# Performance work log

Measured on AMD Instinct MI355X. Metric: run time of the kernel, lower is better.

The kernel has to match this reference:

```python
import jax, jax.numpy as jnp
import numpy as np

B = 131072      # batch
NC = 1000       # num_classes
A = 128         # action_dim
ELD = 128       # embedding_latent_dim
VQN = 512       # vq_num_embeddings
VQD = 64        # vq_embedding_dim
SQUISH = 1.0
CC = 0.25       # commitment cost

def _he(k, fi, fo):
    lim = float(np.sqrt(6.0 / fi))
    return jax.random.uniform(k, (fi, fo), jnp.float32, -lim, lim)

def setup_inputs() -> dict:
    key = jax.random.key(0)
    ks = jax.random.split(key, 16)
    cb_lim = float(np.sqrt(3.0 / VQD))  # variance_scaling fan_in uniform
    return {
        "obs": jax.random.randint(ks[0], (B,), 0, NC),
        "embed": jax.random.normal(ks[1], (NC, ELD), jnp.float32) * 0.02,
        "W1": _he(ks[2], ELD, 128), "b1": jnp.zeros((128,), jnp.float32),
        "W2": _he(ks[3], 128, 128), "b2": jnp.zeros((128,), jnp.float32),
        "W3": _he(ks[4], 128, 128), "b3": jnp.zeros((128,), jnp.float32),
        "Wp": _he(ks[5], 128, VQD), "bp": jnp.zeros((VQD,), jnp.float32),
        "codebook": jax.random.uniform(ks[6], (VQN, VQD), jnp.float32, -cb_lim, cb_lim),
        "Wa": jax.random.normal(ks[7], (VQD, A), jnp.float32) * 0.01, "ba": jnp.zeros((A,), jnp.float32),
        "Ws": jax.random.normal(ks[8], (VQD, A), jnp.float32) * 0.01, "bs": jnp.zeros((A,), jnp.float32),
        "Wc1": _he(ks[9], VQD, 128), "bc1": jnp.zeros((128,), jnp.float32),
        "Wc2": _he(ks[10], 128, 128), "bc2": jnp.zeros((128,), jnp.float32),
        "Wc3": _he(ks[11], 128, 32), "bc3": jnp.zeros((32,), jnp.float32),
        "Wc4": _he(ks[12], 32, 1), "bc4": jnp.zeros((1,), jnp.float32),
    }

def reference(obs, embed, W1, b1, W2, b2, W3, b3, Wp, bp, codebook,
              Wa, ba, Ws, bs, Wc1, bc1, Wc2, bc2, Wc3, bc3, Wc4, bc4):
    # embedding lookup + small dense stack
    y = jnp.take(embed, obs, axis=0)                 # [B, 128]
    z = jax.nn.relu(y @ W1 + b1)
    z = jax.nn.relu(z @ W2 + b2)
    z = jax.nn.relu(z @ W3 + b3)
    z = z @ Wp + bp                                  # [B, 64] project to vq dim
    # VQ: pairwise squared distances, argmin, gather (== one_hot @ codebook)
    d = (jnp.sum(z * z, axis=1, keepdims=True)
         - 2.0 * (z @ codebook.T)
         + jnp.sum(codebook * codebook, axis=1))     # [B, 512]
    idx = jnp.argmin(d, axis=1)                      # [B]
    quant = jnp.take(codebook, idx, axis=0)          # [B, 64]
    q = z + jax.lax.stop_gradient(quant - z)         # straight-through
    e_loss = jnp.mean((jax.lax.stop_gradient(q) - z) ** 2)
    q_loss = jnp.mean((q - jax.lax.stop_gradient(z)) ** 2)
    vq_loss = q_loss + CC * e_loss
    # actor heads (pi = MvNormalDiag(actor_mean, scale_diag); return params)
    actor_mean = jax.nn.sigmoid(q @ Wa + ba)
    scale_diag = jax.nn.sigmoid(q @ Ws + bs) * SQUISH + 1e-8
    # critic head
    c = jax.nn.sigmoid(q @ Wc1 + bc1)
    c = jax.nn.sigmoid(c @ Wc2 + bc2)
    c = jax.nn.sigmoid(c @ Wc3 + bc3)
    critic = jnp.squeeze(c @ Wc4 + bc4, axis=-1)     # [B]
    return actor_mean, scale_diag, critic, vq_loss, idx
```

## Files before the change

kernel.cpp:

```cpp
#include <hip/hip_runtime.h>
#include <math.h>


typedef float f4 __attribute__((ext_vector_type(4)));

__device__ __forceinline__ float sigmoidf_(float x){ return 1.0f/(1.0f + expf(-x)); }

__global__ __launch_bounds__(128) void per_class_kernel(
    const float* __restrict__ embed,
    const float* __restrict__ W1, const float* __restrict__ b1,
    const float* __restrict__ W2, const float* __restrict__ b2,
    const float* __restrict__ W3, const float* __restrict__ b3,
    const float* __restrict__ Wp, const float* __restrict__ bp,
    const float* __restrict__ cb,
    const float* __restrict__ Wa, const float* __restrict__ ba,
    const float* __restrict__ Ws, const float* __restrict__ bs,
    const float* __restrict__ Wc1, const float* __restrict__ bc1,
    const float* __restrict__ Wc2, const float* __restrict__ bc2,
    const float* __restrict__ Wc3, const float* __restrict__ bc3,
    const float* __restrict__ Wc4, const float* __restrict__ bc4,
    float* __restrict__ am_t, float* __restrict__ sd_t,
    float* __restrict__ cr_t, int* __restrict__ idx_t, float* __restrict__ e_t,
    float* __restrict__ loss_slot, int VQN)
{
    const int c = blockIdx.x;
    const int t = threadIdx.x;
    if (c == 0 && t == 0) *loss_slot = 0.0f;

    __shared__ double Abuf[128];
    __shared__ double Bbuf[128];
    __shared__ double zp[64];
    __shared__ float  qv[64];
    __shared__ double rd[128];
    __shared__ int    ri[128];
    __shared__ float  h1[128], h2[128], h3[32];

    Abuf[t] = (double)embed[(size_t)c * 128 + t];
    __syncthreads();

    {
        double a0 = (double)b1[t], a1 = 0.0, a2 = 0.0, a3 = 0.0;
        for (int i = 0; i < 128; i += 4) {
            a0 = fma(Abuf[i+0], (double)W1[(i+0) * 128 + t], a0);
            a1 = fma(Abuf[i+1], (double)W1[(i+1) * 128 + t], a1);
            a2 = fma(Abuf[i+2], (double)W1[(i+2) * 128 + t], a2);
            a3 = fma(Abuf[i+3], (double)W1[(i+3) * 128 + t], a3);
        }
        double acc = (a0 + a1) + (a2 + a3);
        Bbuf[t] = acc > 0.0 ? acc : 0.0;
    }
    __syncthreads();

    {
        double a0 = (double)b2[t], a1 = 0.0, a2 = 0.0, a3 = 0.0;
        for (int i = 0; i < 128; i += 4) {
            a0 = fma(Bbuf[i+0], (double)W2[(i+0) * 128 + t], a0);
            a1 = fma(Bbuf[i+1], (double)W2[(i+1) * 128 + t], a1);
            a2 = fma(Bbuf[i+2], (double)W2[(i+2) * 128 + t], a2);
            a3 = fma(Bbuf[i+3], (double)W2[(i+3) * 128 + t], a3);
        }
        double acc = (a0 + a1) + (a2 + a3);
        Abuf[t] = acc > 0.0 ? acc : 0.0;
    }
    __syncthreads();

    {
        double a0 = (double)b3[t], a1 = 0.0, a2 = 0.0, a3 = 0.0;
        for (int i = 0; i < 128; i += 4) {
            a0 = fma(Abuf[i+0], (double)W3[(i+0) * 128 + t], a0);
            a1 = fma(Abuf[i+1], (double)W3[(i+1) * 128 + t], a1);
            a2 = fma(Abuf[i+2], (double)W3[(i+2) * 128 + t], a2);
            a3 = fma(Abuf[i+3], (double)W3[(i+3) * 128 + t], a3);
        }
        double acc = (a0 + a1) + (a2 + a3);
        Bbuf[t] = acc > 0.0 ? acc : 0.0;
    }
    __syncthreads();

    if (t < 64) {
        double a0 = (double)bp[t], a1 = 0.0, a2 = 0.0, a3 = 0.0;
        for (int i = 0; i < 128; i += 4) {
            a0 = fma(Bbuf[i+0], (double)Wp[(i+0) * 64 + t], a0);
            a1 = fma(Bbuf[i+1], (double)Wp[(i+1) * 64 + t], a1);
            a2 = fma(Bbuf[i+2], (double)Wp[(i+2) * 64 + t], a2);
            a3 = fma(Bbuf[i+3], (double)Wp[(i+3) * 64 + t], a3);
        }
        zp[t] = (a0 + a1) + (a2 + a3);
    }
    __syncthreads();

    double best = 1e300; int bidx = 0;
    for (int k = t; k < VQN; k += 128) {
        const float* crow = cb + (size_t)k * 64;
        double s0 = 0.0, s1 = 0.0;
        for (int j = 0; j < 64; j += 2) {
            double d0 = zp[j+0] - (double)crow[j+0];
            double d1 = zp[j+1] - (double)crow[j+1];
            s0 = fma(d0, d0, s0);
            s1 = fma(d1, d1, s1);
        }
        double s = s0 + s1;
        if (s < best) { best = s; bidx = k; }
    }
    rd[t] = best; ri[t] = bidx;
    __syncthreads();
    for (int sft = 64; sft > 0; sft >>= 1) {
        if (t < sft) {
            if (rd[t + sft] < rd[t] || (rd[t + sft] == rd[t] && ri[t + sft] < ri[t])) {
                rd[t] = rd[t + sft]; ri[t] = ri[t + sft];
            }
        }
        __syncthreads();
    }
    const int widx = ri[0];
    if (t < 64) qv[t] = cb[(size_t)widx * 64 + t];
    __syncthreads();

    {
        float la0 = ba[t],  la1 = 0.0f;
        float ls0 = bs[t],  ls1 = 0.0f;
        float l10 = bc1[t], l11 = 0.0f;
        for (int j = 0; j < 64; j += 2) {
            float q0 = qv[j], q1 = qv[j+1];
            la0 = fmaf(q0, Wa[j * 128 + t], la0);
            la1 = fmaf(q1, Wa[(j+1) * 128 + t], la1);
            ls0 = fmaf(q0, Ws[j * 128 + t], ls0);
            ls1 = fmaf(q1, Ws[(j+1) * 128 + t], ls1);
            l10 = fmaf(q0, Wc1[j * 128 + t], l10);
            l11 = fmaf(q1, Wc1[(j+1) * 128 + t], l11);
        }
        am_t[(size_t)c * 128 + t] = sigmoidf_(la0 + la1);
        sd_t[(size_t)c * 128 + t] = sigmoidf_(ls0 + ls1) * 1.0f + 1e-8f;
        h1[t] = sigmoidf_(l10 + l11);
    }
    __syncthreads();

    {
        float l20 = bc2[t], l21 = 0.0f;
        for (int i = 0; i < 128; i += 2) {
            l20 = fmaf(h1[i],   Wc2[i * 128 + t],     l20);
            l21 = fmaf(h1[i+1], Wc2[(i+1) * 128 + t], l21);
        }
        h2[t] = sigmoidf_(l20 + l21);
    }
    __syncthreads();

    if (t < 32) {
        float l30 = bc3[t], l31 = 0.0f;
        for (int i = 0; i < 128; i += 2) {
            l30 = fmaf(h2[i],   Wc3[i * 32 + t],     l30);
            l31 = fmaf(h2[i+1], Wc3[(i+1) * 32 + t], l31);
        }
        h3[t] = sigmoidf_(l30 + l31);
    }
    __syncthreads();

    if (t == 0) {
        float l4 = bc4[0];
        for (int i = 0; i < 32; ++i) l4 = fmaf(h3[i], Wc4[i], l4);
        cr_t[c] = l4;
        idx_t[c] = widx;
        double e0 = 0.0, e1 = 0.0;
        for (int j = 0; j < 64; j += 2) {
            double d0 = (double)qv[j]   - zp[j];
            double d1 = (double)qv[j+1] - zp[j+1];
            e0 = fma(d0, d0, e0); e1 = fma(d1, d1, e1);
        }
        e_t[c] = (float)(e0 + e1);
    }
}

__global__ __launch_bounds__(256) void scatter_vec_kernel(
    const int* __restrict__ obs,
    const f4* __restrict__ am_t, const f4* __restrict__ sd_t,
    f4* __restrict__ out, int B)
{
    int gid = blockIdx.x * 256 + threadIdx.x;
    int half = B * 32;
    if (gid < half) {
        int b = gid >> 5;
        int j = gid & 31;
        __builtin_nontemporal_store(am_t[(size_t)obs[b] * 32 + j], &out[gid]);
    } else {
        int g = gid - half;
        int b = g >> 5;
        int j = g & 31;
        __builtin_nontemporal_store(sd_t[(size_t)obs[b] * 32 + j], &out[gid]);
    }
}

__global__ __launch_bounds__(256) void scatter_scalar_kernel(
    const int* __restrict__ obs, const float* __restrict__ cr_t,
    const int* __restrict__ idx_t, const float* __restrict__ e_t,
    float* __restrict__ out_critic, float* __restrict__ out_idx,
    float* __restrict__ out_loss, int B, float scale)
{
    int b = blockIdx.x * 256 + threadIdx.x;
    float e = 0.0f;
    if (b < B) {
        int o = obs[b];
        __builtin_nontemporal_store(cr_t[o], &out_critic[b]);
        __builtin_nontemporal_store((float)idx_t[o], &out_idx[b]);
        e = e_t[o];
    }
    __shared__ float red[256];
    red[threadIdx.x] = e;
    __syncthreads();
    for (int s = 128; s > 0; s >>= 1) {
        if (threadIdx.x < s) red[threadIdx.x] += red[threadIdx.x + s];
        __syncthreads();
    }
    if (threadIdx.x == 0) atomicAdd(out_loss, red[0] * scale);
}

extern "C" void kernel_launch(void* const* d_in, const int* in_sizes, int n_in,
                              void* d_out, int out_size, void* d_ws, size_t ws_size,
                              hipStream_t stream)
{
    const int*   obs   = (const int*)  d_in[0];
    const float* embed = (const float*)d_in[1];
    const float* W1    = (const float*)d_in[2];
    const float* b1    = (const float*)d_in[3];
    const float* W2    = (const float*)d_in[4];
    const float* b2    = (const float*)d_in[5];
    const float* W3    = (const float*)d_in[6];
    const float* b3    = (const float*)d_in[7];
    const float* Wp    = (const float*)d_in[8];
    const float* bp    = (const float*)d_in[9];
    const float* cb    = (const float*)d_in[10];
    const float* Wa    = (const float*)d_in[11];
    const float* ba    = (const float*)d_in[12];
    const float* Ws    = (const float*)d_in[13];
    const float* bs    = (const float*)d_in[14];
    const float* Wc1   = (const float*)d_in[15];
    const float* bc1   = (const float*)d_in[16];
    const float* Wc2   = (const float*)d_in[17];
    const float* bc2   = (const float*)d_in[18];
    const float* Wc3   = (const float*)d_in[19];
    const float* bc3   = (const float*)d_in[20];
    const float* Wc4   = (const float*)d_in[21];
    const float* bc4   = (const float*)d_in[22];

    const int B   = in_sizes[0];
    const int NC  = in_sizes[1] / 128;
    const int VQN = in_sizes[10] / 64;

    float* am_t = (float*)d_ws;
    float* sd_t = am_t + (size_t)NC * 128;
    float* cr_t = sd_t + (size_t)NC * 128;
    float* e_t  = cr_t + NC;
    int*   idx_t = (int*)(e_t + NC);

    float* out = (float*)d_out;
    const size_t cr_off   = (size_t)B * 256;
    const size_t loss_off = cr_off + (size_t)B;
    const size_t idx_off  = loss_off + 1;

    per_class_kernel<<<NC, 128, 0, stream>>>(
        embed, W1, b1, W2, b2, W3, b3, Wp, bp, cb,
        Wa, ba, Ws, bs, Wc1, bc1, Wc2, bc2, Wc3, bc3, Wc4, bc4,
        am_t, sd_t, cr_t, idx_t, e_t, out + loss_off, VQN);

    int vec_threads = 2 * B * 32;
    scatter_vec_kernel<<<vec_threads / 256, 256, 0, stream>>>(
        obs, (const f4*)am_t, (const f4*)sd_t, (f4*)out, B);

    scatter_scalar_kernel<<<(B + 255) / 256, 256, 0, stream>>>(
        obs, cr_t, idx_t, e_t, out + cr_off, out + idx_off, out + loss_off,
        B, 1.25f / ((float)B * 64.0f));
}
```

Before: 255.9 us.

## Transpose codebook to double layout and merge scatter kernels into one launch

Adds a pre-pass that transposes the codebook into a column-major double buffer. In the distance loop, each thread then reads coalesced codebook entries for four codes at once, instead of strided row reads with float-to-double conversion. The two scatter kernels are also merged into one launch with block-range dispatch, which removes one kernel launch. In exchange it adds a transpose kernel launch and extra workspace, and the double buffer doubles the bytes read for the codebook.

```diff
diff --git a/kernel.cpp b/kernel.cpp
--- a/kernel.cpp
+++ b/kernel.cpp
@@ -5,6 +5,18 @@
 typedef float f4 __attribute__((ext_vector_type(4)));
 
 __device__ __forceinline__ float sigmoidf_(float x){ return 1.0f/(1.0f + expf(-x)); }
+
+__global__ __launch_bounds__(256) void transpose_cb_kernel(
+    const float* __restrict__ cb, double* __restrict__ cbT, int VQN)
+{
+    int gid = blockIdx.x * 256 + threadIdx.x;
+    int total = 64 * VQN;
+    if (gid < total) {
+        int j = gid / VQN;
+        int k = gid - j * VQN;
+        cbT[gid] = (double)cb[(size_t)k * 64 + j];
+    }
+}
 
 __global__ __launch_bounds__(128) void per_class_kernel(
     const float* __restrict__ embed,
@@ -12,7 +24,7 @@
     const float* __restrict__ W2, const float* __restrict__ b2,
     const float* __restrict__ W3, const float* __restrict__ b3,
     const float* __restrict__ Wp, const float* __restrict__ bp,
-    const float* __restrict__ cb,
+    const float* __restrict__ cb, const double* __restrict__ cbT,
     const float* __restrict__ Wa, const float* __restrict__ ba,
     const float* __restrict__ Ws, const float* __restrict__ bs,
     const float* __restrict__ Wc1, const float* __restrict__ bc1,
@@ -90,17 +102,42 @@
     __syncthreads();
 
     double best = 1e300; int bidx = 0;
-    for (int k = t; k < VQN; k += 128) {
-        const float* crow = cb + (size_t)k * 64;
-        double s0 = 0.0, s1 = 0.0;
+    if (VQN == 512) {
+        const double* base = cbT + t;
+        double a0e = 0.0, a0o = 0.0, a1e = 0.0, a1o = 0.0;
+        double a2e = 0.0, a2o = 0.0, a3e = 0.0, a3o = 0.0;
         for (int j = 0; j < 64; j += 2) {
-            double d0 = zp[j+0] - (double)crow[j+0];
-            double d1 = zp[j+1] - (double)crow[j+1];
-            s0 = fma(d0, d0, s0);
-            s1 = fma(d1, d1, s1);
-        }
-        double s = s0 + s1;
-        if (s < best) { best = s; bidx = k; }
+            const double* r0 = base + (size_t)j * 512;
+            const double* r1 = r0 + 512;
+            double z0 = zp[j], z1 = zp[j+1];
+            double d;
+            d = z0 - r0[0];    a0e = fma(d, d, a0e);
+            d = z1 - r1[0];    a0o = fma(d, d, a0o);
+            d = z0 - r0[128];  a1e = fma(d, d, a1e);
+            d = z1 - r1[128];  a1o = fma(d, d, a1o);
+            d = z0 - r0[256];  a2e = fma(d, d, a2e);
+            d = z1 - r1[256];  a2o = fma(d, d, a2o);
+            d = z0 - r0[384];  a3e = fma(d, d, a3e);
+            d = z1 - r1[384];  a3o = fma(d, d, a3o);
+        }
+        double s0 = a0e + a0o, s1 = a1e + a1o, s2 = a2e + a2o, s3 = a3e + a3o;
+        best = s0; bidx = t;
+        if (s1 < best) { best = s1; bidx = t + 128; }
+        if (s2 < best) { best = s2; bidx = t + 256; }
+        if (s3 < best) { best = s3; bidx = t + 384; }
+    } else {
+        for (int k = t; k < VQN; k += 128) {
+            const float* crow = cb + (size_t)k * 64;
+            double s0 = 0.0, s1 = 0.0;
+            for (int j = 0; j < 64; j += 2) {
+                double d0 = zp[j+0] - (double)crow[j+0];
+                double d1 = zp[j+1] - (double)crow[j+1];
+                s0 = fma(d0, d0, s0);
+                s1 = fma(d1, d1, s1);
+            }
+            double s = s0 + s1;
+            if (s < best) { best = s; bidx = k; }
+        }
     }
     rd[t] = best; ri[t] = bidx;
     __syncthreads();
@@ -170,32 +207,33 @@
     }
 }
 
-__global__ __launch_bounds__(256) void scatter_vec_kernel(
+__global__ __launch_bounds__(256) void scatter_kernel(
     const int* __restrict__ obs,
     const f4* __restrict__ am_t, const f4* __restrict__ sd_t,
-    f4* __restrict__ out, int B)
+    const float* __restrict__ cr_t, const int* __restrict__ idx_t,
+    const float* __restrict__ e_t,
+    f4* __restrict__ out_vec, float* __restrict__ out_critic,
+    float* __restrict__ out_idx, float* __restrict__ out_loss,
+    int B, float scale)
 {
-    int gid = blockIdx.x * 256 + threadIdx.x;
-    int half = B * 32;
-    if (gid < half) {
-        int b = gid >> 5;
-        int j = gid & 31;
-        __builtin_nontemporal_store(am_t[(size_t)obs[b] * 32 + j], &out[gid]);
-    } else {
-        int g = gid - half;
-        int b = g >> 5;
-        int j = g & 31;
-        __builtin_nontemporal_store(sd_t[(size_t)obs[b] * 32 + j], &out[gid]);
-    }
-}
-
-__global__ __launch_bounds__(256) void scatter_scalar_kernel(
-    const int* __restrict__ obs, const float* __restrict__ cr_t,
-    const int* __restrict__ idx_t, const float* __restrict__ e_t,
-    float* __restrict__ out_critic, float* __restrict__ out_idx,
-    float* __restrict__ out_loss, int B, float scale)
-{
-    int b = blockIdx.x * 256 + threadIdx.x;
+    __shared__ float red[256];
+    const int vecBlocks = (2 * B * 32) / 256;
+    if ((int)blockIdx.x < vecBlocks) {
+        int gid = blockIdx.x * 256 + threadIdx.x;
+        int half = B * 32;
+        if (gid < half) {
+            int b = gid >> 5;
+            int j = gid & 31;
+            __builtin_nontemporal_store(am_t[(size_t)obs[b] * 32 + j], &out_vec[gid]);
+        } else {
+            int g = gid - half;
+            int b = g >> 5;
+            int j = g & 31;
+            __builtin_nontemporal_store(sd_t[(size_t)obs[b] * 32 + j], &out_vec[gid]);
+        }
+        return;
+    }
+    int b = (blockIdx.x - vecBlocks) * 256 + threadIdx.x;
     float e = 0.0f;
     if (b < B) {
         int o = obs[b];
@@ -203,7 +241,6 @@
         __builtin_nontemporal_store((float)idx_t[o], &out_idx[b]);
         e = e_t[o];
     }
-    __shared__ float red[256];
     red[threadIdx.x] = e;
     __syncthreads();
     for (int s = 128; s > 0; s >>= 1) {
@@ -245,27 +282,29 @@
     const int NC  = in_sizes[1] / 128;
     const int VQN = in_sizes[10] / 64;
 
-    float* am_t = (float*)d_ws;
-    float* sd_t = am_t + (size_t)NC * 128;
-    float* cr_t = sd_t + (size_t)NC * 128;
-    float* e_t  = cr_t + NC;
-    int*   idx_t = (int*)(e_t + NC);
+    double* cbT  = (double*)d_ws;
+    float*  am_t = (float*)(cbT + (size_t)64 * VQN);
+    float*  sd_t = am_t + (size_t)NC * 128;
+    float*  cr_t = sd_t + (size_t)NC * 128;
+    float*  e_t  = cr_t + NC;
+    int*    idx_t = (int*)(e_t + NC);
 
     float* out = (float*)d_out;
     const size_t cr_off   = (size_t)B * 256;
     const size_t loss_off = cr_off + (size_t)B;
     const size_t idx_off  = loss_off + 1;
 
+    transpose_cb_kernel<<<(64 * VQN + 255) / 256, 256, 0, stream>>>(cb, cbT, VQN);
+
     per_class_kernel<<<NC, 128, 0, stream>>>(
-        embed, W1, b1, W2, b2, W3, b3, Wp, bp, cb,
+        embed, W1, b1, W2, b2, W3, b3, Wp, bp, cb, cbT,
         Wa, ba, Ws, bs, Wc1, bc1, Wc2, bc2, Wc3, bc3, Wc4, bc4,
         am_t, sd_t, cr_t, idx_t, e_t, out + loss_off, VQN);
 
-    int vec_threads = 2 * B * 32;
-    scatter_vec_kernel<<<vec_threads / 256, 256, 0, stream>>>(
-        obs, (const f4*)am_t, (const f4*)sd_t, (f4*)out, B);
-
-    scatter_scalar_kernel<<<(B + 255) / 256, 256, 0, stream>>>(
-        obs, cr_t, idx_t, e_t, out + cr_off, out + idx_off, out + loss_off,
+    const int vecBlocks    = (2 * B * 32) / 256;
+    const int scalarBlocks = (B + 255) / 256;
+    scatter_kernel<<<vecBlocks + scalarBlocks, 256, 0, stream>>>(
+        obs, (const f4*)am_t, (const f4*)sd_t, cr_t, idx_t, e_t,
+        (f4*)out, out + cr_off, out + idx_off, out + loss_off,
         B, 1.25f / ((float)B * 64.0f));
 }
```

Result: no change. 257.1 us (+0.4%).

## Process two classes per block and merge scatter kernels into one launch

Applied to the files above, without the earlier changes.

The per-class kernel now handles two classes per block, so each weight and codebook value loaded from global memory is reused for two FMAs. The two scatter kernels are merged into one launch, where each vec thread writes both the am and sd rows, and trailing blocks handle the scalar outputs and the loss reduction. This cuts weight-load traffic, launch count and block count, but halves the number of per-class blocks, to 500 on a GPU with many CUs, and raises register and shared-memory use per block.

```diff
diff --git a/kernel.cpp b/kernel.cpp
--- a/kernel.cpp
+++ b/kernel.cpp
@@ -21,181 +21,242 @@
     const float* __restrict__ Wc4, const float* __restrict__ bc4,
     float* __restrict__ am_t, float* __restrict__ sd_t,
     float* __restrict__ cr_t, int* __restrict__ idx_t, float* __restrict__ e_t,
-    float* __restrict__ loss_slot, int VQN)
+    float* __restrict__ loss_slot, int VQN, int NC)
 {
-    const int c = blockIdx.x;
-    const int t = threadIdx.x;
-    if (c == 0 && t == 0) *loss_slot = 0.0f;
-
-    __shared__ double Abuf[128];
-    __shared__ double Bbuf[128];
-    __shared__ double zp[64];
-    __shared__ float  qv[64];
-    __shared__ double rd[128];
-    __shared__ int    ri[128];
-    __shared__ float  h1[128], h2[128], h3[32];
-
-    Abuf[t] = (double)embed[(size_t)c * 128 + t];
-    __syncthreads();
-
-    {
-        double a0 = (double)b1[t], a1 = 0.0, a2 = 0.0, a3 = 0.0;
+    const int t  = threadIdx.x;
+    const int c0 = blockIdx.x * 2;
+    const int c1 = (c0 + 1 < NC) ? c0 + 1 : NC - 1;
+    if (blockIdx.x == 0 && t == 0) *loss_slot = 0.0f;
+
+    __shared__ double A0[128], A1[128];
+    __shared__ double B0[128], B1[128];
+    __shared__ double zp0[64], zp1[64];
+    __shared__ float  qv0[64], qv1[64];
+    __shared__ double rdA[128], rdB[128];
+    __shared__ int    riA[128], riB[128];
+    __shared__ float  h1a[128], h1b[128], h2a[128], h2b[128], h3a[32], h3b[32];
+
+    A0[t] = (double)embed[(size_t)c0 * 128 + t];
+    A1[t] = (double)embed[(size_t)c1 * 128 + t];
+    __syncthreads();
+
+    {
+        double bb = (double)b1[t];
+        double aA0 = bb, aA1 = 0.0, aA2 = 0.0, aA3 = 0.0;
+        double aB0 = bb, aB1 = 0.0, aB2 = 0.0, aB3 = 0.0;
         for (int i = 0; i < 128; i += 4) {
-            a0 = fma(Abuf[i+0], (double)W1[(i+0) * 128 + t], a0);
-            a1 = fma(Abuf[i+1], (double)W1[(i+1) * 128 + t], a1);
-            a2 = fma(Abuf[i+2], (double)W1[(i+2) * 128 + t], a2);
-            a3 = fma(Abuf[i+3], (double)W1[(i+3) * 128 + t], a3);
-        }
-        double acc = (a0 + a1) + (a2 + a3);
-        Bbuf[t] = acc > 0.0 ? acc : 0.0;
-    }
-    __syncthreads();
-
-    {
-        double a0 = (double)b2[t], a1 = 0.0, a2 = 0.0, a3 = 0.0;
+            double w0 = (double)W1[(i+0) * 128 + t];
+            double w1 = (double)W1[(i+1) * 128 + t];
+            double w2 = (double)W1[(i+2) * 128 + t];
+            double w3 = (double)W1[(i+3) * 128 + t];
+            aA0 = fma(A0[i+0], w0, aA0);  aB0 = fma(A1[i+0], w0, aB0);
+            aA1 = fma(A0[i+1], w1, aA1);  aB1 = fma(A1[i+1], w1, aB1);
+            aA2 = fma(A0[i+2], w2, aA2);  aB2 = fma(A1[i+2], w2, aB2);
+            aA3 = fma(A0[i+3], w3, aA3);  aB3 = fma(A1[i+3], w3, aB3);
+        }
+        double accA = (aA0 + aA1) + (aA2 + aA3);
+        double accB = (aB0 + aB1) + (aB2 + aB3);
+        B0[t] = accA > 0.0 ? accA : 0.0;
+        B1[t] = accB > 0.0 ? accB : 0.0;
+    }
+    __syncthreads();
+
+    {
+        double bb = (double)b2[t];
+        double aA0 = bb, aA1 = 0.0, aA2 = 0.0, aA3 = 0.0;
+        double aB0 = bb, aB1 = 0.0, aB2 = 0.0, aB3 = 0.0;
         for (int i = 0; i < 128; i += 4) {
-            a0 = fma(Bbuf[i+0], (double)W2[(i+0) * 128 + t], a0);
-            a1 = fma(Bbuf[i+1], (double)W2[(i+1) * 128 + t], a1);
-            a2 = fma(Bbuf[i+2], (double)W2[(i+2) * 128 + t], a2);
-            a3 = fma(Bbuf[i+3], (double)W2[(i+3) * 128 + t], a3);
-        }
-        double acc = (a0 + a1) + (a2 + a3);
-        Abuf[t] = acc > 0.0 ? acc : 0.0;
-    }
-    __syncthreads();
-
-    {
-        double a0 = (double)b3[t], a1 = 0.0, a2 = 0.0, a3 = 0.0;
+            double w0 = (double)W2[(i+0) * 128 + t];
+            double w1 = (double)W2[(i+1) * 128 + t];
+            double w2 = (double)W2[(i+2) * 128 + t];
+            double w3 = (double)W2[(i+3) * 128 + t];
+            aA0 = fma(B0[i+0], w0, aA0);  aB0 = fma(B1[i+0], w0, aB0);
+            aA1 = fma(B0[i+1], w1, aA1);  aB1 = fma(B1[i+1], w1, aB1);
+            aA2 = fma(B0[i+2], w2, aA2);  aB2 = fma(B1[i+2], w2, aB2);
+            aA3 = fma(B0[i+3], w3, aA3);  aB3 = fma(B1[i+3], w3, aB3);
+        }
+        double accA = (aA0 + aA1) + (aA2 + aA3);
+        double accB = (aB0 + aB1) + (aB2 + aB3);
+        A0[t] = accA > 0.0 ? accA : 0.0;
+        A1[t] = accB > 0.0 ? accB : 0.0;
+    }
+    __syncthreads();
+
+    {
+        double bb = (double)b3[t];
+        double aA0 = bb, aA1 = 0.0, aA2 = 0.0, aA3 = 0.0;
+        double aB0 = bb, aB1 = 0.0, aB2 = 0.0, aB3 = 0.0;
         for (int i = 0; i < 128; i += 4) {
-            a0 = fma(Abuf[i+0], (double)W3[(i+0) * 128 + t], a0);
-            a1 = fma(Abuf[i+1], (double)W3[(i+1) * 128 + t], a1);
-            a2 = fma(Abuf[i+2], (double)W3[(i+2) * 128 + t], a2);
-            a3 = fma(Abuf[i+3], (double)W3[(i+3) * 128 + t], a3);
-        }
-        double acc = (a0 + a1) + (a2 + a3);
-        Bbuf[t] = acc > 0.0 ? acc : 0.0;
+            double w0 = (double)W3[(i+0) * 128 + t];
+            double w1 = (double)W3[(i+1) * 128 + t];
+            double w2 = (double)W3[(i+2) * 128 + t];
+            double w3 = (double)W3[(i+3) * 128 + t];
+            aA0 = fma(A0[i+0], w0, aA0);  aB0 = fma(A1[i+0], w0, aB0);
+            aA1 = fma(A0[i+1], w1, aA1);  aB1 = fma(A1[i+1], w1, aB1);
+            aA2 = fma(A0[i+2], w2, aA2);  aB2 = fma(A1[i+2], w2, aB2);
+            aA3 = fma(A0[i+3], w3, aA3);  aB3 = fma(A1[i+3], w3, aB3);
+        }
+        double accA = (aA0 + aA1) + (aA2 + aA3);
+        double accB = (aB0 + aB1) + (aB2 + aB3);
+        B0[t] = accA > 0.0 ? accA : 0.0;
+        B1[t] = accB > 0.0 ? accB : 0.0;
     }
     __syncthreads();
 
     if (t < 64) {
-        double a0 = (double)bp[t], a1 = 0.0, a2 = 0.0, a3 = 0.0;
+        double bb = (double)bp[t];
+        double aA0 = bb, aA1 = 0.0, aA2 = 0.0, aA3 = 0.0;
+        double aB0 = bb, aB1 = 0.0, aB2 = 0.0, aB3 = 0.0;
         for (int i = 0; i < 128; i += 4) {
-            a0 = fma(Bbuf[i+0], (double)Wp[(i+0) * 64 + t], a0);
-            a1 = fma(Bbuf[i+1], (double)Wp[(i+1) * 64 + t], a1);
-            a2 = fma(Bbuf[i+2], (double)Wp[(i+2) * 64 + t], a2);
-            a3 = fma(Bbuf[i+3], (double)Wp[(i+3) * 64 + t], a3);
-        }
-        zp[t] = (a0 + a1) + (a2 + a3);
-    }
-    __syncthreads();
-
-    double best = 1e300; int bidx = 0;
+            double w0 = (double)Wp[(i+0) * 64 + t];
+            double w1 = (double)Wp[(i+1) * 64 + t];
+            double w2 = (double)Wp[(i+2) * 64 + t];
+            double w3 = (double)Wp[(i+3) * 64 + t];
+            aA0 = fma(B0[i+0], w0, aA0);  aB0 = fma(B1[i+0], w0, aB0);
+            aA1 = fma(B0[i+1], w1, aA1);  aB1 = fma(B1[i+1], w1, aB1);
+            aA2 = fma(B0[i+2], w2, aA2);  aB2 = fma(B1[i+2], w2, aB2);
+            aA3 = fma(B0[i+3], w3, aA3);  aB3 = fma(B1[i+3], w3, aB3);
+        }
+        zp0[t] = (aA0 + aA1) + (aA2 + aA3);
+        zp1[t] = (aB0 + aB1) + (aB2 + aB3);
+    }
+    __syncthreads();
+
+    double bestA = 1e300, bestB = 1e300; int biA = 0, biB = 0;
     for (int k = t; k < VQN; k += 128) {
         const float* crow = cb + (size_t)k * 64;
-        double s0 = 0.0, s1 = 0.0;
+        double sA0 = 0.0, sA1 = 0.0, sB0 = 0.0, sB1 = 0.0;
         for (int j = 0; j < 64; j += 2) {
-            double d0 = zp[j+0] - (double)crow[j+0];
-            double d1 = zp[j+1] - (double)crow[j+1];
-            s0 = fma(d0, d0, s0);
-            s1 = fma(d1, d1, s1);
-        }
-        double s = s0 + s1;
-        if (s < best) { best = s; bidx = k; }
-    }
-    rd[t] = best; ri[t] = bidx;
+            double w0 = (double)crow[j+0];
+            double w1 = (double)crow[j+1];
+            double dA0 = zp0[j+0] - w0, dA1 = zp0[j+1] - w1;
+            double dB0 = zp1[j+0] - w0, dB1 = zp1[j+1] - w1;
+            sA0 = fma(dA0, dA0, sA0);  sA1 = fma(dA1, dA1, sA1);
+            sB0 = fma(dB0, dB0, sB0);  sB1 = fma(dB1, dB1, sB1);
+        }
+        double sA = sA0 + sA1, sB = sB0 + sB1;
+        if (sA < bestA) { bestA = sA; biA = k; }
+        if (sB < bestB) { bestB = sB; biB = k; }
+    }
+    rdA[t] = bestA; riA[t] = biA;
+    rdB[t] = bestB; riB[t] = biB;
     __syncthreads();
     for (int sft = 64; sft > 0; sft >>= 1) {
         if (t < sft) {
-            if (rd[t + sft] < rd[t] || (rd[t + sft] == rd[t] && ri[t + sft] < ri[t])) {
-                rd[t] = rd[t + sft]; ri[t] = ri[t + sft];
+            if (rdA[t + sft] < rdA[t] || (rdA[t + sft] == rdA[t] && riA[t + sft] < riA[t])) {
+                rdA[t] = rdA[t + sft]; riA[t] = riA[t + sft];
             }
+            if (rdB[t + sft] < rdB[t] || (rdB[t + sft] == rdB[t] && riB[t + sft] < riB[t])) {
+                rdB[t] = rdB[t + sft]; riB[t] = riB[t + sft];
+            }
         }
         __syncthreads();
     }
-    const int widx = ri[0];
-    if (t < 64) qv[t] = cb[(size_t)widx * 64 + t];
-    __syncthreads();
-
-    {
-        float la0 = ba[t],  la1 = 0.0f;
-        float ls0 = bs[t],  ls1 = 0.0f;
-        float l10 = bc1[t], l11 = 0.0f;
+    const int widxA = riA[0];
+    const int widxB = riB[0];
+    if (t < 64) qv0[t] = cb[(size_t)widxA * 64 + t];
+    else        qv1[t - 64] = cb[(size_t)widxB * 64 + (t - 64)];
+    __syncthreads();
+
+    {
+        float la_A0 = ba[t],  la_A1 = 0.0f, la_B0 = ba[t],  la_B1 = 0.0f;
+        float ls_A0 = bs[t],  ls_A1 = 0.0f, ls_B0 = bs[t],  ls_B1 = 0.0f;
+        float l1_A0 = bc1[t], l1_A1 = 0.0f, l1_B0 = bc1[t], l1_B1 = 0.0f;
         for (int j = 0; j < 64; j += 2) {
-            float q0 = qv[j], q1 = qv[j+1];
-            la0 = fmaf(q0, Wa[j * 128 + t], la0);
-            la1 = fmaf(q1, Wa[(j+1) * 128 + t], la1);
-            ls0 = fmaf(q0, Ws[j * 128 + t], ls0);
-            ls1 = fmaf(q1, Ws[(j+1) * 128 + t], ls1);
-            l10 = fmaf(q0, Wc1[j * 128 + t], l10);
-            l11 = fmaf(q1, Wc1[(j+1) * 128 + t], l11);
-        }
-        am_t[(size_t)c * 128 + t] = sigmoidf_(la0 + la1);
-        sd_t[(size_t)c * 128 + t] = sigmoidf_(ls0 + ls1) * 1.0f + 1e-8f;
-        h1[t] = sigmoidf_(l10 + l11);
-    }
-    __syncthreads();
-
-    {
-        float l20 = bc2[t], l21 = 0.0f;
+            float wa0 = Wa[j * 128 + t],  wa1 = Wa[(j+1) * 128 + t];
+            float ws0 = Ws[j * 128 + t],  ws1 = Ws[(j+1) * 128 + t];
+            float wc0 = Wc1[j * 128 + t], wc1 = Wc1[(j+1) * 128 + t];
+            float qA0 = qv0[j], qA1 = qv0[j+1];
+            float qB0 = qv1[j], qB1 = qv1[j+1];
+            la_A0 = fmaf(qA0, wa0, la_A0);  la_A1 = fmaf(qA1, wa1, la_A1);
+            la_B0 = fmaf(qB0, wa0, la_B0);  la_B1 = fmaf(qB1, wa1, la_B1);
+            ls_A0 = fmaf(qA0, ws0, ls_A0);  ls_A1 = fmaf(qA1, ws1, ls_A1);
+            ls_B0 = fmaf(qB0, ws0, ls_B0);  ls_B1 = fmaf(qB1, ws1, ls_B1);
+            l1_A0 = fmaf(qA0, wc0, l1_A0);  l1_A1 = fmaf(qA1, wc1, l1_A1);
+            l1_B0 = fmaf(qB0, wc0, l1_B0);  l1_B1 = fmaf(qB1, wc1, l1_B1);
+        }
+        am_t[(size_t)c0 * 128 + t] = sigmoidf_(la_A0 + la_A1);
+        am_t[(size_t)c1 * 128 + t] = sigmoidf_(la_B0 + la_B1);
+        sd_t[(size_t)c0 * 128 + t] = sigmoidf_(ls_A0 + ls_A1) * 1.0f + 1e-8f;
+        sd_t[(size_t)c1 * 128 + t] = sigmoidf_(ls_B0 + ls_B1) * 1.0f + 1e-8f;
+        h1a[t] = sigmoidf_(l1_A0 + l1_A1);
+        h1b[t] = sigmoidf_(l1_B0 + l1_B1);
+    }
+    __syncthreads();
+
+    {
+        float lA0 = bc2[t], lA1 = 0.0f, lB0 = bc2[t], lB1 = 0.0f;
         for (int i = 0; i < 128; i += 2) {
-            l20 = fmaf(h1[i],   Wc2[i * 128 + t],     l20);
-            l21 = fmaf(h1[i+1], Wc2[(i+1) * 128 + t], l21);
-        }
-        h2[t] = sigmoidf_(l20 + l21);
+            float w0 = Wc2[i * 128 + t], w1 = Wc2[(i+1) * 128 + t];
+            lA0 = fmaf(h1a[i],   w0, lA0);  lA1 = fmaf(h1a[i+1], w1, lA1);
+            lB0 = fmaf(h1b[i],   w0, lB0);  lB1 = fmaf(h1b[i+1], w1, lB1);
+        }
+        h2a[t] = sigmoidf_(lA0 + lA1);
+        h2b[t] = sigmoidf_(lB0 + lB1);
     }
     __syncthreads();
 
     if (t < 32) {
-        float l30 = bc3[t], l31 = 0.0f;
+        float lA0 = bc3[t], lA1 = 0.0f, lB0 = bc3[t], lB1 = 0.0f;
         for (int i = 0; i < 128; i += 2) {
-            l30 = fmaf(h2[i],   Wc3[i * 32 + t],     l30);
-            l31 = fmaf(h2[i+1], Wc3[(i+1) * 32 + t], l31);
-        }
-        h3[t] = sigmoidf_(l30 + l31);
+            float w0 = Wc3[i * 32 + t], w1 = Wc3[(i+1) * 32 + t];
+            lA0 = fmaf(h2a[i],   w0, lA0);  lA1 = fmaf(h2a[i+1], w1, lA1);
+            lB0 = fmaf(h2b[i],   w0, lB0);  lB1 = fmaf(h2b[i+1], w1, lB1);
+        }
+        h3a[t] = sigmoidf_(lA0 + lA1);
+        h3b[t] = sigmoidf_(lB0 + lB1);
     }
     __syncthreads();
 
     if (t == 0) {
         float l4 = bc4[0];
-        for (int i = 0; i < 32; ++i) l4 = fmaf(h3[i], Wc4[i], l4);
-        cr_t[c] = l4;
-        idx_t[c] = widx;
+        for (int i = 0; i < 32; ++i) l4 = fmaf(h3a[i], Wc4[i], l4);
+        cr_t[c0] = l4;
+        idx_t[c0] = widxA;
         double e0 = 0.0, e1 = 0.0;
         for (int j = 0; j < 64; j += 2) {
-            double d0 = (double)qv[j]   - zp[j];
-            double d1 = (double)qv[j+1] - zp[j+1];
+            double d0 = (double)qv0[j]   - zp0[j];
+            double d1 = (double)qv0[j+1] - zp0[j+1];
             e0 = fma(d0, d0, e0); e1 = fma(d1, d1, e1);
         }
-        e_t[c] = (float)(e0 + e1);
+        e_t[c0] = (float)(e0 + e1);
+    }
+    if (t == 64 && c1 != c0) {
+        float l4 = bc4[0];
+        for (int i = 0; i < 32; ++i) l4 = fmaf(h3b[i], Wc4[i], l4);
+        cr_t[c1] = l4;
+        idx_t[c1] = widxB;
+        double e0 = 0.0, e1 = 0.0;
+        for (int j = 0; j < 64; j += 2) {
+            double d0 = (double)qv1[j]   - zp1[j];
+            double d1 = (double)qv1[j+1] - zp1[j+1];
+            e0 = fma(d0, d0, e0); e1 = fma(d1, d1, e1);
+        }
+        e_t[c1] = (float)(e0 + e1);
     }
 }
 
-__global__ __launch_bounds__(256) void scatter_vec_kernel(
+__global__ __launch_bounds__(256) void scatter_kernel(
     const int* __restrict__ obs,
     const f4* __restrict__ am_t, const f4* __restrict__ sd_t,
-    f4* __restrict__ out, int B)
+    const float* __restrict__ cr_t, const int* __restrict__ idx_t,
+    const float* __restrict__ e_t,
+    f4* __restrict__ out_vec, float* __restrict__ out_critic,
+    float* __restrict__ out_idx, float* __restrict__ out_loss,
+    int B, float scale)
 {
-    int gid = blockIdx.x * 256 + threadIdx.x;
-    int half = B * 32;
-    if (gid < half) {
+    __shared__ float red[256];
+    const int vecBlocks = (B * 32) / 256;
+    if ((int)blockIdx.x < vecBlocks) {
+        int gid = blockIdx.x * 256 + threadIdx.x;
         int b = gid >> 5;
         int j = gid & 31;
-        __builtin_nontemporal_store(am_t[(size_t)obs[b] * 32 + j], &out[gid]);
-    } else {
-        int g = gid - half;
-        int b = g >> 5;
-        int j = g & 31;
-        __builtin_nontemporal_store(sd_t[(size_t)obs[b] * 32 + j], &out[gid]);
-    }
-}
-
-__global__ __launch_bounds__(256) void scatter_scalar_kernel(
-    const int* __restrict__ obs, const float* __restrict__ cr_t,
-    const int* __restrict__ idx_t, const float* __restrict__ e_t,
-    float* __restrict__ out_critic, float* __restrict__ out_idx,
-    float* __restrict__ out_loss, int B, float scale)
-{
-    int b = blockIdx.x * 256 + threadIdx.x;
+        size_t row = (size_t)obs[b] * 32 + j;
+        __builtin_nontemporal_store(am_t[row], &out_vec[gid]);
+        __builtin_nontemporal_store(sd_t[row], &out_vec[(size_t)B * 32 + gid]);
+        return;
+    }
+    int b = (blockIdx.x - vecBlocks) * 256 + threadIdx.x;
     float e = 0.0f;
     if (b < B) {
         int o = obs[b];
@@ -203,7 +264,6 @@
         __builtin_nontemporal_store((float)idx_t[o], &out_idx[b]);
         e = e_t[o];
     }
-    __shared__ float red[256];
     red[threadIdx.x] = e;
     __syncthreads();
     for (int s = 128; s > 0; s >>= 1) {
@@ -256,16 +316,15 @@
     const size_t loss_off = cr_off + (size_t)B;
     const size_t idx_off  = loss_off + 1;
 
-    per_class_kernel<<<NC, 128, 0, stream>>>(
+    per_class_kernel<<<(NC + 1) / 2, 128, 0, stream>>>(
         embed, W1, b1, W2, b2, W3, b3, Wp, bp, cb,
         Wa, ba, Ws, bs, Wc1, bc1, Wc2, bc2, Wc3, bc3, Wc4, bc4,
-        am_t, sd_t, cr_t, idx_t, e_t, out + loss_off, VQN);
-
-    int vec_threads = 2 * B * 32;
-    scatter_vec_kernel<<<vec_threads / 256, 256, 0, stream>>>(
-        obs, (const f4*)am_t, (const f4*)sd_t, (f4*)out, B);
-
-    scatter_scalar_kernel<<<(B + 255) / 256, 256, 0, stream>>>(
-        obs, cr_t, idx_t, e_t, out + cr_off, out + idx_off, out + loss_off,
+        am_t, sd_t, cr_t, idx_t, e_t, out + loss_off, VQN, NC);
+
+    const int vecBlocks    = (B * 32) / 256;
+    const int scalarBlocks = (B + 255) / 256;
+    scatter_kernel<<<vecBlocks + scalarBlocks, 256, 0, stream>>>(
+        obs, (const f4*)am_t, (const f4*)sd_t, cr_t, idx_t, e_t,
+        (f4*)out, out + cr_off, out + idx_off, out + loss_off,
         B, 1.25f / ((float)B * 64.0f));
 }
```

Result: slower. 267.1 us (+4.4%).

## Vectorize per-class MLP weight loads with split-K and merge scatter kernels

Applied to the files above, without the earlier changes.

Rewrites the per-class MLP layers so each thread loads float4 (or float2) weight slices and computes four outputs over a quarter of the input dimension, with partial sums reduced through shared memory. The VQ argmin reduction now uses wavefront shuffles instead of a shared-memory tree. The two scatter kernels are merged into one launch, where each vector thread writes both the actor-mean and scale rows. The goal is fewer load instructions, fewer barriers and one less launch, at the cost of extra shared-memory partial buffers and syncs.

```diff
diff --git a/kernel.cpp b/kernel.cpp
--- a/kernel.cpp
+++ b/kernel.cpp
@@ -3,6 +3,7 @@
 
 
 typedef float f4 __attribute__((ext_vector_type(4)));
+typedef float f2 __attribute__((ext_vector_type(2)));
 
 __device__ __forceinline__ float sigmoidf_(float x){ return 1.0f/(1.0f + expf(-x)); }
 
@@ -27,132 +28,194 @@
     const int t = threadIdx.x;
     if (c == 0 && t == 0) *loss_slot = 0.0f;
 
-    __shared__ double Abuf[128];
-    __shared__ double Bbuf[128];
+    __shared__ double Ain[128], Bin[128];
+    __shared__ double part[4][128];
     __shared__ double zp[64];
     __shared__ float  qv[64];
-    __shared__ double rd[128];
-    __shared__ int    ri[128];
+    __shared__ double rds[2];
+    __shared__ int    ris[2];
+    __shared__ int    widx_s;
+    __shared__ float  fpart[4][128];
+    __shared__ float  gpart[2][128];
     __shared__ float  h1[128], h2[128], h3[32];
 
-    Abuf[t] = (double)embed[(size_t)c * 128 + t];
-    __syncthreads();
-
-    {
-        double a0 = (double)b1[t], a1 = 0.0, a2 = 0.0, a3 = 0.0;
-        for (int i = 0; i < 128; i += 4) {
-            a0 = fma(Abuf[i+0], (double)W1[(i+0) * 128 + t], a0);
-            a1 = fma(Abuf[i+1], (double)W1[(i+1) * 128 + t], a1);
-            a2 = fma(Abuf[i+2], (double)W1[(i+2) * 128 + t], a2);
-            a3 = fma(Abuf[i+3], (double)W1[(i+3) * 128 + t], a3);
-        }
-        double acc = (a0 + a1) + (a2 + a3);
-        Bbuf[t] = acc > 0.0 ? acc : 0.0;
-    }
-    __syncthreads();
-
-    {
-        double a0 = (double)b2[t], a1 = 0.0, a2 = 0.0, a3 = 0.0;
-        for (int i = 0; i < 128; i += 4) {
-            a0 = fma(Bbuf[i+0], (double)W2[(i+0) * 128 + t], a0);
-            a1 = fma(Bbuf[i+1], (double)W2[(i+1) * 128 + t], a1);
-            a2 = fma(Bbuf[i+2], (double)W2[(i+2) * 128 + t], a2);
-            a3 = fma(Bbuf[i+3], (double)W2[(i+3) * 128 + t], a3);
-        }
-        double acc = (a0 + a1) + (a2 + a3);
-        Abuf[t] = acc > 0.0 ? acc : 0.0;
-    }
-    __syncthreads();
-
-    {
-        double a0 = (double)b3[t], a1 = 0.0, a2 = 0.0, a3 = 0.0;
-        for (int i = 0; i < 128; i += 4) {
-            a0 = fma(Abuf[i+0], (double)W3[(i+0) * 128 + t], a0);
-            a1 = fma(Abuf[i+1], (double)W3[(i+1) * 128 + t], a1);
-            a2 = fma(Abuf[i+2], (double)W3[(i+2) * 128 + t], a2);
-            a3 = fma(Abuf[i+3], (double)W3[(i+3) * 128 + t], a3);
-        }
-        double acc = (a0 + a1) + (a2 + a3);
-        Bbuf[t] = acc > 0.0 ? acc : 0.0;
-    }
-    __syncthreads();
+    const int q4 = (t & 31) << 2;
+    const int h  = t >> 5;
+
+    Ain[t] = (double)embed[(size_t)c * 128 + t];
+    __syncthreads();
+
+#define TRUNK_LAYER(W, B, IN, OUT)                                          \
+    {                                                                       \
+        double a0 = (h == 0) ? (double)B[q4+0] : 0.0;                       \
+        double a1 = (h == 0) ? (double)B[q4+1] : 0.0;                       \
+        double a2 = (h == 0) ? (double)B[q4+2] : 0.0;                       \
+        double a3 = (h == 0) ? (double)B[q4+3] : 0.0;                       \
+        for (int s = 0; s < 32; ++s) {                                      \
+            int i = h + (s << 2);                                           \
+            f4 w = *(const f4*)(W + (size_t)i * 128 + q4);                  \
+            double x = IN[i];                                               \
+            a0 = fma(x, (double)w.x, a0);                                   \
+            a1 = fma(x, (double)w.y, a1);                                   \
+            a2 = fma(x, (double)w.z, a2);                                   \
+            a3 = fma(x, (double)w.w, a3);                                   \
+        }                                                                   \
+        part[h][q4+0] = a0; part[h][q4+1] = a1;                             \
+        part[h][q4+2] = a2; part[h][q4+3] = a3;                             \
+    }                                                                       \
+    __syncthreads();                                                        \
+    {                                                                       \
+        double acc = (part[0][t] + part[1][t]) + (part[2][t] + part[3][t]); \
+        OUT[t] = acc > 0.0 ? acc : 0.0;                                     \
+    }                                                                       \
+    __syncthreads();
+
+    TRUNK_LAYER(W1, b1, Ain, Bin)
+    TRUNK_LAYER(W2, b2, Bin, Ain)
+    TRUNK_LAYER(W3, b3, Ain, Bin)
+#undef TRUNK_LAYER
 
     if (t < 64) {
-        double a0 = (double)bp[t], a1 = 0.0, a2 = 0.0, a3 = 0.0;
-        for (int i = 0; i < 128; i += 4) {
-            a0 = fma(Bbuf[i+0], (double)Wp[(i+0) * 64 + t], a0);
-            a1 = fma(Bbuf[i+1], (double)Wp[(i+1) * 64 + t], a1);
-            a2 = fma(Bbuf[i+2], (double)Wp[(i+2) * 64 + t], a2);
-            a3 = fma(Bbuf[i+3], (double)Wp[(i+3) * 64 + t], a3);
-        }
-        zp[t] = (a0 + a1) + (a2 + a3);
-    }
+        const int q4p = (t & 15) << 2;
+        const int hp  = t >> 4;
+        double a0 = (hp == 0) ? (double)bp[q4p+0] : 0.0;
+        double a1 = (hp == 0) ? (double)bp[q4p+1] : 0.0;
+        double a2 = (hp == 0) ? (double)bp[q4p+2] : 0.0;
+        double a3 = (hp == 0) ? (double)bp[q4p+3] : 0.0;
+        for (int s = 0; s < 32; ++s) {
+            int i = hp + (s << 2);
+            f4 w = *(const f4*)(Wp + (size_t)i * 64 + q4p);
+            double x = Bin[i];
+            a0 = fma(x, (double)w.x, a0);
+            a1 = fma(x, (double)w.y, a1);
+            a2 = fma(x, (double)w.z, a2);
+            a3 = fma(x, (double)w.w, a3);
+        }
+        part[hp][q4p+0] = a0; part[hp][q4p+1] = a1;
+        part[hp][q4p+2] = a2; part[hp][q4p+3] = a3;
+    }
+    __syncthreads();
+    if (t < 64) zp[t] = (part[0][t] + part[1][t]) + (part[2][t] + part[3][t]);
     __syncthreads();
 
     double best = 1e300; int bidx = 0;
     for (int k = t; k < VQN; k += 128) {
         const float* crow = cb + (size_t)k * 64;
         double s0 = 0.0, s1 = 0.0;
-        for (int j = 0; j < 64; j += 2) {
-            double d0 = zp[j+0] - (double)crow[j+0];
-            double d1 = zp[j+1] - (double)crow[j+1];
-            s0 = fma(d0, d0, s0);
-            s1 = fma(d1, d1, s1);
+        for (int j = 0; j < 64; j += 4) {
+            f4 v = *(const f4*)(crow + j);
+            double d0 = zp[j+0] - (double)v.x;
+            double d1 = zp[j+1] - (double)v.y;
+            double d2 = zp[j+2] - (double)v.z;
+            double d3 = zp[j+3] - (double)v.w;
+            s0 = fma(d0, d0, s0);  s1 = fma(d1, d1, s1);
+            s0 = fma(d2, d2, s0);  s1 = fma(d3, d3, s1);
         }
         double s = s0 + s1;
         if (s < best) { best = s; bidx = k; }
     }
-    rd[t] = best; ri[t] = bidx;
-    __syncthreads();
-    for (int sft = 64; sft > 0; sft >>= 1) {
-        if (t < sft) {
-            if (rd[t + sft] < rd[t] || (rd[t + sft] == rd[t] && ri[t + sft] < ri[t])) {
-                rd[t] = rd[t + sft]; ri[t] = ri[t + sft];
-            }
-        }
-        __syncthreads();
-    }
-    const int widx = ri[0];
+    for (int off = 32; off > 0; off >>= 1) {
+        double od = __shfl_down(best, off);
+        int    oi = __shfl_down(bidx, off);
+        if (od < best || (od == best && oi < bidx)) { best = od; bidx = oi; }
+    }
+    if ((t & 63) == 0) { rds[t >> 6] = best; ris[t >> 6] = bidx; }
+    __syncthreads();
+    if (t == 0) {
+        double b0 = rds[0]; int i0 = ris[0];
+        if (rds[1] < b0 || (rds[1] == b0 && ris[1] < i0)) { i0 = ris[1]; }
+        widx_s = i0;
+    }
+    __syncthreads();
+    const int widx = widx_s;
     if (t < 64) qv[t] = cb[(size_t)widx * 64 + t];
     __syncthreads();
 
     {
-        float la0 = ba[t],  la1 = 0.0f;
-        float ls0 = bs[t],  ls1 = 0.0f;
-        float l10 = bc1[t], l11 = 0.0f;
-        for (int j = 0; j < 64; j += 2) {
-            float q0 = qv[j], q1 = qv[j+1];
-            la0 = fmaf(q0, Wa[j * 128 + t], la0);
-            la1 = fmaf(q1, Wa[(j+1) * 128 + t], la1);
-            ls0 = fmaf(q0, Ws[j * 128 + t], ls0);
-            ls1 = fmaf(q1, Ws[(j+1) * 128 + t], ls1);
-            l10 = fmaf(q0, Wc1[j * 128 + t], l10);
-            l11 = fmaf(q1, Wc1[(j+1) * 128 + t], l11);
-        }
-        am_t[(size_t)c * 128 + t] = sigmoidf_(la0 + la1);
-        sd_t[(size_t)c * 128 + t] = sigmoidf_(ls0 + ls1) * 1.0f + 1e-8f;
-        h1[t] = sigmoidf_(l10 + l11);
-    }
+        const int m  = t >> 6;
+        const int hh = (t >> 5) & 1;
+        const float* Wm = m ? Ws : Wa;
+        const float* bm = m ? bs : ba;
+        float a0 = hh ? 0.0f : bm[q4+0];
+        float a1 = hh ? 0.0f : bm[q4+1];
+        float a2 = hh ? 0.0f : bm[q4+2];
+        float a3 = hh ? 0.0f : bm[q4+3];
+        for (int s = 0; s < 32; ++s) {
+            int j = hh + (s << 1);
+            f4 w = *(const f4*)(Wm + (size_t)j * 128 + q4);
+            float qj = qv[j];
+            a0 = fmaf(qj, w.x, a0);
+            a1 = fmaf(qj, w.y, a1);
+            a2 = fmaf(qj, w.z, a2);
+            a3 = fmaf(qj, w.w, a3);
+        }
+        fpart[t >> 5][q4+0] = a0; fpart[t >> 5][q4+1] = a1;
+        fpart[t >> 5][q4+2] = a2; fpart[t >> 5][q4+3] = a3;
+    }
+    __syncthreads();
+
+    if (t < 64) {
+        const int hh = t >> 5;
+        float a0 = hh ? 0.0f : bc1[q4+0];
+        float a1 = hh ? 0.0f : bc1[q4+1];
+        float a2 = hh ? 0.0f : bc1[q4+2];
+        float a3 = hh ? 0.0f : bc1[q4+3];
+        for (int s = 0; s < 32; ++s) {
+            int j = hh + (s << 1);
+            f4 w = *(const f4*)(Wc1 + (size_t)j * 128 + q4);
+            float qj = qv[j];
+            a0 = fmaf(qj, w.x, a0);
+            a1 = fmaf(qj, w.y, a1);
+            a2 = fmaf(qj, w.z, a2);
+            a3 = fmaf(qj, w.w, a3);
+        }
+        gpart[hh][q4+0] = a0; gpart[hh][q4+1] = a1;
+        gpart[hh][q4+2] = a2; gpart[hh][q4+3] = a3;
+    } else {
+        int o = (t - 64) << 1;
+        am_t[(size_t)c * 128 + o]     = sigmoidf_(fpart[0][o]   + fpart[1][o]);
+        am_t[(size_t)c * 128 + o + 1] = sigmoidf_(fpart[0][o+1] + fpart[1][o+1]);
+        sd_t[(size_t)c * 128 + o]     = sigmoidf_(fpart[2][o]   + fpart[3][o])   * 1.0f + 1e-8f;
+        sd_t[(size_t)c * 128 + o + 1] = sigmoidf_(fpart[2][o+1] + fpart[3][o+1]) * 1.0f + 1e-8f;
+    }
+    __syncthreads();
+    h1[t] = sigmoidf_(gpart[0][t] + gpart[1][t]);
     __syncthreads();
 
     {
-        float l20 = bc2[t], l21 = 0.0f;
-        for (int i = 0; i < 128; i += 2) {
-            l20 = fmaf(h1[i],   Wc2[i * 128 + t],     l20);
-            l21 = fmaf(h1[i+1], Wc2[(i+1) * 128 + t], l21);
-        }
-        h2[t] = sigmoidf_(l20 + l21);
-    }
+        const int o2 = (t & 63) << 1;
+        const int hh = t >> 6;
+        float a0 = hh ? 0.0f : bc2[o2+0];
+        float a1 = hh ? 0.0f : bc2[o2+1];
+        for (int s = 0; s < 64; ++s) {
+            int i = hh + (s << 1);
+            f2 w = *(const f2*)(Wc2 + (size_t)i * 128 + o2);
+            float x = h1[i];
+            a0 = fmaf(x, w.x, a0);
+            a1 = fmaf(x, w.y, a1);
+        }
+        gpart[hh][o2+0] = a0; gpart[hh][o2+1] = a1;
+    }
+    __syncthreads();
+    h2[t] = sigmoidf_(gpart[0][t] + gpart[1][t]);
     __syncthreads();
 
     if (t < 32) {
-        float l30 = bc3[t], l31 = 0.0f;
-        for (int i = 0; i < 128; i += 2) {
-            l30 = fmaf(h2[i],   Wc3[i * 32 + t],     l30);
-            l31 = fmaf(h2[i+1], Wc3[(i+1) * 32 + t], l31);
-        }
-        h3[t] = sigmoidf_(l30 + l31);
-    }
+        const int o2 = (t & 15) << 1;
+        const int hh = t >> 4;
+        float a0 = hh ? 0.0f : bc3[o2+0];
+        float a1 = hh ? 0.0f : bc3[o2+1];
+        for (int s = 0; s < 64; ++s) {
+            int i = hh + (s << 1);
+            f2 w = *(const f2*)(Wc3 + (size_t)i * 32 + o2);
+            float x = h2[i];
+            a0 = fmaf(x, w.x, a0);
+            a1 = fmaf(x, w.y, a1);
+        }
+        gpart[hh][o2+0] = a0; gpart[hh][o2+1] = a1;
+    }
+    __syncthreads();
+    if (t < 32) h3[t] = sigmoidf_(gpart[0][t] + gpart[1][t]);
     __syncthreads();
 
     if (t == 0) {
@@ -170,32 +233,27 @@
     }
 }
 
-__global__ __launch_bounds__(256) void scatter_vec_kernel(
+__global__ __launch_bounds__(256) void scatter_kernel(
     const int* __restrict__ obs,
     const f4* __restrict__ am_t, const f4* __restrict__ sd_t,
-    f4* __restrict__ out, int B)
+    const float* __restrict__ cr_t, const int* __restrict__ idx_t,
+    const float* __restrict__ e_t,
+    f4* __restrict__ out_vec, float* __restrict__ out_critic,
+    float* __restrict__ out_idx, float* __restrict__ out_loss,
+    int B, float scale)
 {
-    int gid = blockIdx.x * 256 + threadIdx.x;
-    int half = B * 32;
-    if (gid < half) {
+    __shared__ float red[256];
+    const int vecBlocks = (B * 32) / 256;
+    if ((int)blockIdx.x < vecBlocks) {
+        int gid = blockIdx.x * 256 + threadIdx.x;
         int b = gid >> 5;
         int j = gid & 31;
-        __builtin_nontemporal_store(am_t[(size_t)obs[b] * 32 + j], &out[gid]);
-    } else {
-        int g = gid - half;
-        int b = g >> 5;
-        int j = g & 31;
-        __builtin_nontemporal_store(sd_t[(size_t)obs[b] * 32 + j], &out[gid]);
-    }
-}
-
-__global__ __launch_bounds__(256) void scatter_scalar_kernel(
-    const int* __restrict__ obs, const float* __restrict__ cr_t,
-    const int* __restrict__ idx_t, const float* __restrict__ e_t,
-    float* __restrict__ out_critic, float* __restrict__ out_idx,
-    float* __restrict__ out_loss, int B, float scale)
-{
-    int b = blockIdx.x * 256 + threadIdx.x;
+        size_t row = (size_t)obs[b] * 32 + j;
+        __builtin_nontemporal_store(am_t[row], &out_vec[gid]);
+        __builtin_nontemporal_store(sd_t[row], &out_vec[(size_t)B * 32 + gid]);
+        return;
+    }
+    int b = (blockIdx.x - vecBlocks) * 256 + threadIdx.x;
     float e = 0.0f;
     if (b < B) {
         int o = obs[b];
@@ -203,7 +261,6 @@
         __builtin_nontemporal_store((float)idx_t[o], &out_idx[b]);
         e = e_t[o];
     }
-    __shared__ float red[256];
     red[threadIdx.x] = e;
     __syncthreads();
     for (int s = 128; s > 0; s >>= 1) {
@@ -261,11 +318,10 @@
         Wa, ba, Ws, bs, Wc1, bc1, Wc2, bc2, Wc3, bc3, Wc4, bc4,
         am_t, sd_t, cr_t, idx_t, e_t, out + loss_off, VQN);
 
-    int vec_threads = 2 * B * 32;
-    scatter_vec_kernel<<<vec_threads / 256, 256, 0, stream>>>(
-        obs, (const f4*)am_t, (const f4*)sd_t, (f4*)out, B);
-
-    scatter_scalar_kernel<<<(B + 255) / 256, 256, 0, stream>>>(
-        obs, cr_t, idx_t, e_t, out + cr_off, out + idx_off, out + loss_off,
+    const int vecBlocks    = (B * 32) / 256;
+    const int scalarBlocks = (B + 255) / 256;
+    scatter_kernel<<<vecBlocks + scalarBlocks, 256, 0, stream>>>(
+        obs, (const f4*)am_t, (const f4*)sd_t, cr_t, idx_t, e_t,
+        (f4*)out, out + cr_off, out + idx_off, out + loss_off,
         B, 1.25f / ((float)B * 64.0f));
 }
```

Measured after the change: 240.4 us. 1.06x faster.
